# Optimization experiments

Hardware: AMD Instinct MI355X
Metric: run time of the kernel (lower is better)

The kernel has to match this reference:

```python
import jax, jax.numpy as jnp
import numpy as np

D_MODEL = 1024
N_HEADS = 16
HEAD_DIM = D_MODEL // N_HEADS


def setup_inputs() -> dict:
    key = jax.random.key(0)
    ks = jax.random.split(key, 5)
    B, S = 2, 2048
    x = jax.random.normal(ks[0], (B, S, D_MODEL), dtype=jnp.float32)
    # nn.Linear weights: [out_features, in_features]
    s_in = 1.0 / np.sqrt(D_MODEL)
    qkv_w = jax.random.uniform(ks[1], (3 * D_MODEL, D_MODEL), jnp.float32, -s_in, s_in)
    qkv_b = jax.random.uniform(ks[2], (3 * D_MODEL,), jnp.float32, -s_in, s_in)
    out_w = jax.random.uniform(ks[3], (D_MODEL, D_MODEL), jnp.float32, -s_in, s_in)
    out_b = jax.random.uniform(ks[4], (D_MODEL,), jnp.float32, -s_in, s_in)
    return {"x": x, "qkv_w": qkv_w, "qkv_b": qkv_b, "out_w": out_w, "out_b": out_b}


def reference(x, qkv_w, qkv_b, out_w, out_b):
    B, S, D = x.shape
    H, Hd = N_HEADS, HEAD_DIM
    scale = 1.0 / np.sqrt(Hd)
    qkv = jnp.einsum('bsd,ed->bse', x, qkv_w) + qkv_b  # [B,S,3D]
    qkv = qkv.reshape(B, S, 3, H, Hd)
    q = qkv[:, :, 0].transpose(0, 2, 1, 3)  # [B,H,S,Hd]
    k = qkv[:, :, 1].transpose(0, 2, 1, 3)
    v = qkv[:, :, 2].transpose(0, 2, 1, 3)
    scores = jnp.einsum('bhqd,bhkd->bhqk', q, k) * scale  # [B,H,S,S]
    causal = jnp.triu(jnp.ones((S, S), dtype=bool), k=1)
    scores = jnp.where(causal[None, None], -jnp.inf, scores)
    probs = jax.nn.softmax(scores, axis=-1)
    out = jnp.einsum('bhqk,bhkd->bhqd', probs, v)  # [B,H,S,Hd]
    out = out.transpose(0, 2, 1, 3).reshape(B, S, D)
    out = jnp.einsum('bsd,ed->bse', out, out_w) + out_b
    return out
```

## Files before the change

kernel.cpp:

```cpp
#include <hip/hip_runtime.h>
#include <hip/hip_bf16.h>

#define SEQ    2048
#define DMODEL 1024
#define NHEAD  16
#define HDIM   64
#define BATCH  2
#define NTOK   (BATCH * SEQ)

#define N_X   (NTOK * DMODEL)
#define N_WQ  (3 * DMODEL * DMODEL)
#define N_BQ  (3 * DMODEL)
#define N_WO  (DMODEL * DMODEL)
#define N_BO  (DMODEL)
#define N_CANON (N_X + N_WQ + N_BQ + N_WO + N_BO)

#define NEG_SENT (-1.0e30f)
#define QSCALE 0.1803368801111f

typedef __attribute__((ext_vector_type(8))) short short8;
typedef __attribute__((ext_vector_type(4))) short short4v;
typedef __attribute__((ext_vector_type(4))) float f32x4;

#define MFMA_BF16(A, B, C) __builtin_amdgcn_mfma_f32_16x16x32_bf16((A), (B), (C), 0, 0, 0)

static __device__ __forceinline__ short8 load8(const __hip_bfloat16* p) {
    return *(const short8*)p;
}

static __device__ __forceinline__ void async16(const void* g, void* l) {
    __builtin_amdgcn_global_load_lds(
        (const __attribute__((address_space(1))) unsigned int*)g,
        (__attribute__((address_space(3))) unsigned int*)l,
        16, 0, 0);
}

__global__ void detect_kernel(const unsigned short* __restrict__ w, int* flag) {
    int cnt = 0;
    for (int i = threadIdx.x; i < 512; i += 64) {
        const unsigned e = (w[i] >> 7) & 0xFF;
        if (e >= 125) cnt++;
    }
#pragma unroll
    for (int o = 32; o; o >>= 1) cnt += __shfl_down(cnt, o);
    if (threadIdx.x == 0) *flag = (cnt > 8) ? 1 : 0;
}

__global__ __launch_bounds__(256) void canon_kernel(
    const void* __restrict__ s0, const void* __restrict__ s1,
    const void* __restrict__ s2, const void* __restrict__ s3,
    const void* __restrict__ s4,
    __hip_bfloat16* __restrict__ dst, const int* __restrict__ flag)
{
    const int v = blockIdx.x * 256 + threadIdx.x;
    if (v >= N_CANON / 8) return;
    const int idx = v * 8;
    const void* src;
    int off;
    if (idx < N_X)                          { src = s0; off = idx; }
    else if (idx < N_X + N_WQ)              { src = s1; off = idx - N_X; }
    else if (idx < N_X + N_WQ + N_BQ)       { src = s2; off = idx - (N_X + N_WQ); }
    else if (idx < N_X + N_WQ + N_BQ + N_WO){ src = s3; off = idx - (N_X + N_WQ + N_BQ); }
    else                                    { src = s4; off = idx - (N_X + N_WQ + N_BQ + N_WO); }
    if (*flag != 0) {
        const f32x4* sp = (const f32x4*)((const float*)src + off);
        const f32x4 x0 = sp[0], x1 = sp[1];
        short8 o;
#pragma unroll
        for (int j = 0; j < 4; ++j) {
            o[j]     = (short)__bfloat16_as_ushort(__float2bfloat16(x0[j]));
            o[4 + j] = (short)__bfloat16_as_ushort(__float2bfloat16(x1[j]));
        }
        *(short8*)&dst[idx] = o;
    } else {
        *(short8*)&dst[idx] = *(const short8*)((const __hip_bfloat16*)src + off);
    }
}

__global__ __launch_bounds__(256) void qkv_gemm_kernel(
    const __hip_bfloat16* __restrict__ X,
    const __hip_bfloat16* __restrict__ W,
    const __hip_bfloat16* __restrict__ bias,
    __hip_bfloat16* __restrict__ Qs,
    __hip_bfloat16* __restrict__ Kb,
    __hip_bfloat16* __restrict__ Vt)
{
    constexpr int Kd = DMODEL;
    __shared__ __align__(16) __hip_bfloat16 As[3][128 * 32];
    __shared__ __align__(16) __hip_bfloat16 Bs[3][128 * 32];

    const int tid   = threadIdx.x;
    const int lane  = tid & 63;
    const int w     = tid >> 6;
    const int mTile = blockIdx.y * 128;
    const int nTile = blockIdx.x * 128;
    const int wm    = (w >> 1) * 64;
    const int wn    = (w & 1) * 64;
    const int lm    = lane & 15;
    const int q4    = lane >> 4;
    const int lks   = (q4 ^ ((lm >> 1) & 3)) * 8;

    f32x4 acc[4][4];
#pragma unroll
    for (int i = 0; i < 4; ++i)
#pragma unroll
        for (int j = 0; j < 4; ++j)
            acc[i][j] = (f32x4){0.f, 0.f, 0.f, 0.f};

    const int r0c = tid >> 2;
    const int r1c = (tid + 256) >> 2;
    const int cbs = ((tid & 3) ^ ((tid >> 3) & 3)) * 8;

    const __hip_bfloat16* gA0 = &X[(size_t)(mTile + r0c) * Kd + cbs];
    const __hip_bfloat16* gA1 = &X[(size_t)(mTile + r1c) * Kd + cbs];
    const __hip_bfloat16* gB0 = &W[(size_t)(nTile + r0c) * Kd + cbs];
    const __hip_bfloat16* gB1 = &W[(size_t)(nTile + r1c) * Kd + cbs];

    async16(gA0, (char*)As[0] + tid * 16);
    async16(gA1, (char*)As[0] + tid * 16 + 4096);
    async16(gB0, (char*)Bs[0] + tid * 16);
    async16(gB1, (char*)Bs[0] + tid * 16 + 4096);
    async16(gA0 + 32, (char*)As[1] + tid * 16);
    async16(gA1 + 32, (char*)As[1] + tid * 16 + 4096);
    async16(gB0 + 32, (char*)Bs[1] + tid * 16);
    async16(gB1 + 32, (char*)Bs[1] + tid * 16 + 4096);

    int cur = 0;
    constexpr int NIT = Kd / 32;
    for (int it = 0; it < NIT; ++it) {
        if (it + 1 < NIT) {
            asm volatile("s_waitcnt vmcnt(4)" ::: "memory");
        } else {
            asm volatile("s_waitcnt vmcnt(0)" ::: "memory");
        }
        __builtin_amdgcn_s_barrier();
        __builtin_amdgcn_sched_barrier(0);

        if (it + 2 < NIT) {
            const int slot = (cur + 2 >= 3) ? cur - 1 : cur + 2;
            const int k2 = (it + 2) * 32;
            async16(gA0 + k2, (char*)As[slot] + tid * 16);
            async16(gA1 + k2, (char*)As[slot] + tid * 16 + 4096);
            async16(gB0 + k2, (char*)Bs[slot] + tid * 16);
            async16(gB1 + k2, (char*)Bs[slot] + tid * 16 + 4096);
        }

        const __hip_bfloat16* Ac = As[cur];
        const __hip_bfloat16* Bc = Bs[cur];
        short8 a[4], b[4];
#pragma unroll
        for (int i = 0; i < 4; ++i)
            a[i] = *(const short8*)&Ac[(wm + i * 16 + lm) * 32 + lks];
#pragma unroll
        for (int j = 0; j < 4; ++j)
            b[j] = *(const short8*)&Bc[(wn + j * 16 + lm) * 32 + lks];
#pragma unroll
        for (int i = 0; i < 4; ++i)
#pragma unroll
            for (int j = 0; j < 4; ++j)
                acc[i][j] = MFMA_BF16(a[i], b[j], acc[i][j]);

        cur = (cur + 1 == 3) ? 0 : cur + 1;
    }

    const int r0 = (lane >> 4) * 4;
#pragma unroll
    for (int j = 0; j < 4; ++j) {
        const int n  = nTile + wn + j * 16 + lm;
        const float bv = __bfloat162float(bias[n]);
        const int c = n >> 10;
        const int h = (n >> 6) & 15;
        const int d = n & 63;
#pragma unroll
        for (int i = 0; i < 4; ++i) {
            if (c == 2) {
                const int m0 = mTile + wm + i * 16 + r0;
                const int bb = m0 >> 11;
                const int s0 = m0 & (SEQ - 1);
                const int bh = bb * NHEAD + h;
                short4v pk;
#pragma unroll
                for (int r = 0; r < 4; ++r)
                    pk[r] = (short)__bfloat16_as_ushort(
                        __float2bfloat16(acc[i][j][r] + bv));
                *(short4v*)&Vt[(size_t)(bh * HDIM + d) * SEQ + s0] = pk;
            } else {
#pragma unroll
                for (int r = 0; r < 4; ++r) {
                    const int m  = mTile + wm + i * 16 + r0 + r;
                    const int bb = m >> 11;
                    const int s  = m & (SEQ - 1);
                    const int bh = bb * NHEAD + h;
                    const float v = acc[i][j][r] + bv;
                    if (c == 0) {
                        Qs[(size_t)(bh * SEQ + s) * HDIM + d] = __float2bfloat16(v * QSCALE);
                    } else {
                        Kb[(size_t)(bh * SEQ + s) * HDIM + d] = __float2bfloat16(v);
                    }
                }
            }
        }
    }
}

#define P_PITCH 72
__global__ __launch_bounds__(256, 3) void attn_kernel(
    const __hip_bfloat16* __restrict__ Qs,
    const __hip_bfloat16* __restrict__ Kb,
    const __hip_bfloat16* __restrict__ Vt,
    float* __restrict__ Opart,
    float* __restrict__ MLpart)
{
    __shared__ __align__(16) __hip_bfloat16 Kt[2][64 * 64];
    __shared__ __align__(16) __hip_bfloat16 Vs[2][64 * 64];
    __shared__ __align__(16) __hip_bfloat16 Pall[4][32 * P_PITCH];

    const int tid  = threadIdx.x;
    const int lane = tid & 63;
    const int wv   = tid >> 6;
    const int bh   = blockIdx.x;
    const int py   = blockIdx.y;
    const int p    = py / 3;
    const int j3   = py % 3;

    const int c_lo = (j3 == 0) ? 0 : (j3 == 1 ? 12 : 23);
    const int c_hi = (j3 == 0) ? 12 : (j3 == 1 ? 23 : 34);
    const int bnd  = 32 - 2 * p;

    const int lm  = lane & 15;
    const int q4  = lane >> 4;
    const int lk  = q4 * 8;
    const int swz = (lm & 3) << 4;

    __hip_bfloat16* P = Pall[wv];

    const __hip_bfloat16* Qbh = Qs + (size_t)bh * SEQ * HDIM;
    const __hip_bfloat16* Kbh = Kb + (size_t)bh * SEQ * HDIM;
    const __hip_bfloat16* Vbh = Vt + (size_t)bh * HDIM * SEQ;

    const int srow0 = tid >> 3;
    const int scb   = (tid & 7) ^ (srow0 & 7);

    for (int seg = 0; seg < 2; ++seg) {
        int qb, a, b, slot;
        if (seg == 0) {
            if (j3 == 2 && p >= 5) continue;
            qb = 15 - p; a = c_lo;
            b  = (c_hi < bnd) ? c_hi : bnd;
            slot = j3;
        } else {
            if (j3 == 0 || (j3 == 1 && p <= 4)) continue;
            qb = p;
            a  = ((c_lo > bnd) ? c_lo : bnd) - bnd;
            b  = c_hi - bnd;
            slot = (j3 == 2) ? 3 : 4;
        }

        const int wbase = qb * 128 + wv * 32;

        short8 qa[2][2];
#pragma unroll
        for (int i = 0; i < 2; ++i)
#pragma unroll
            for (int h = 0; h < 2; ++h)
                qa[i][h] = load8(&Qbh[(size_t)(wbase + i * 16 + lm) * HDIM + h * 32 + lk]);

        float m_run[2] = {NEG_SENT, NEG_SENT};
        float l_run[2] = {0.f, 0.f};
        f32x4 Oacc[2][4];
#pragma unroll
        for (int i = 0; i < 2; ++i)
#pragma unroll
            for (int t = 0; t < 4; ++t) Oacc[i][t] = (f32x4){0.f, 0.f, 0.f, 0.f};

        __builtin_amdgcn_s_barrier();

        {
            const int kk0 = a * 64;
            async16(&Kbh[(size_t)(kk0 + srow0) * HDIM + scb * 8],      (char*)Kt[0] + tid * 16);
            async16(&Kbh[(size_t)(kk0 + srow0 + 32) * HDIM + scb * 8], (char*)Kt[0] + tid * 16 + 4096);
            async16(&Vbh[(size_t)srow0 * SEQ + kk0 + scb * 8],         (char*)Vs[0] + tid * 16);
            async16(&Vbh[(size_t)(srow0 + 32) * SEQ + kk0 + scb * 8],  (char*)Vs[0] + tid * 16 + 4096);
            if (a + 1 < b) {
                const int kk1 = kk0 + 64;
                async16(&Kbh[(size_t)(kk1 + srow0) * HDIM + scb * 8],      (char*)Kt[1] + tid * 16);
                async16(&Kbh[(size_t)(kk1 + srow0 + 32) * HDIM + scb * 8], (char*)Kt[1] + tid * 16 + 4096);
                async16(&Vbh[(size_t)srow0 * SEQ + kk1 + scb * 8],         (char*)Vs[1] + tid * 16);
                async16(&Vbh[(size_t)(srow0 + 32) * SEQ + kk1 + scb * 8],  (char*)Vs[1] + tid * 16 + 4096);
            }
        }

        int cur = 0;
        for (int ci = a; ci < b; ++ci) {
            const int k0 = ci * 64;

            if (ci + 1 < b) {
                asm volatile("s_waitcnt vmcnt(4)" ::: "memory");
            } else {
                asm volatile("s_waitcnt vmcnt(0)" ::: "memory");
            }
            __builtin_amdgcn_s_barrier();
            __builtin_amdgcn_sched_barrier(0);

            if (k0 <= wbase + 31) {
                const __hip_bfloat16* Kc = Kt[cur];
                const __hip_bfloat16* Vc = Vs[cur];

                short8 ka[4][2];
#pragma unroll
                for (int t = 0; t < 4; ++t)
#pragma unroll
                    for (int h = 0; h < 2; ++h)
                        ka[t][h] = *(const short8*)&Kc[(t * 16 + lm) * 64 +
                                                       (((h * 4 + q4) ^ (lm & 7)) * 8)];

                f32x4 sc[2][4];
#pragma unroll
                for (int i = 0; i < 2; ++i)
#pragma unroll
                    for (int t = 0; t < 4; ++t) sc[i][t] = (f32x4){0.f, 0.f, 0.f, 0.f};
#pragma unroll
                for (int t = 0; t < 4; ++t)
#pragma unroll
                    for (int i = 0; i < 2; ++i) {
                        sc[i][t] = MFMA_BF16(ka[t][0], qa[i][0], sc[i][t]);
                        sc[i][t] = MFMA_BF16(ka[t][1], qa[i][1], sc[i][t]);
                    }

                if (k0 + 63 > wbase) {
#pragma unroll
                    for (int i = 0; i < 2; ++i) {
                        const int row = wbase + i * 16 + lm;
#pragma unroll
                        for (int t = 0; t < 4; ++t)
#pragma unroll
                            for (int r = 0; r < 4; ++r) {
                                const int key = k0 + t * 16 + q4 * 4 + r;
                                if (key > row) sc[i][t][r] = NEG_SENT;
                            }
                    }
                }

#pragma unroll
                for (int i = 0; i < 2; ++i) {
                    float mx = sc[i][0][0];
#pragma unroll
                    for (int t = 0; t < 4; ++t)
#pragma unroll
                        for (int r = 0; r < 4; ++r) mx = fmaxf(mx, sc[i][t][r]);
                    mx = fmaxf(mx, __shfl_xor(mx, 16));
                    mx = fmaxf(mx, __shfl_xor(mx, 32));

                    if (!__all(mx <= m_run[i] + 8.0f)) {
                        const float mn = fmaxf(m_run[i], mx);
                        const float alpha = exp2f(m_run[i] - mn);
                        m_run[i] = mn;
                        l_run[i] *= alpha;
#pragma unroll
                        for (int r = 0; r < 4; ++r) {
                            const float av = __shfl(alpha, q4 * 4 + r);
#pragma unroll
                            for (int t = 0; t < 4; ++t) Oacc[i][t][r] *= av;
                        }
                    }

                    float s = 0.f;
#pragma unroll
                    for (int t = 0; t < 4; ++t)
#pragma unroll
                        for (int r = 0; r < 4; ++r) {
                            const float pv = exp2f(sc[i][t][r] - m_run[i]);
                            sc[i][t][r] = pv;
                            s += pv;
                        }
                    s += __shfl_xor(s, 16);
                    s += __shfl_xor(s, 32);
                    l_run[i] += s;
                }

#pragma unroll
                for (int i = 0; i < 2; ++i)
#pragma unroll
                    for (int t = 0; t < 4; ++t) {
                        short4v pk;
#pragma unroll
                        for (int r = 0; r < 4; ++r)
                            pk[r] = (short)__bfloat16_as_ushort(__float2bfloat16(sc[i][t][r]));
                        const int col = (t * 16 + q4 * 4) ^ swz;
                        *(short4v*)&P[(i * 16 + lm) * P_PITCH + col] = pk;
                    }

#pragma unroll
                for (int h = 0; h < 2; ++h) {
                    short8 pa[2];
#pragma unroll
                    for (int i = 0; i < 2; ++i)
                        pa[i] = *(const short8*)&P[(i * 16 + lm) * P_PITCH + ((h * 32 + lk) ^ swz)];
#pragma unroll
                    for (int t = 0; t < 4; ++t) {
                        const short8 vb = *(const short8*)&Vc[(t * 16 + lm) * 64 +
                                                              (((h * 4 + q4) ^ (lm & 7)) * 8)];
#pragma unroll
                        for (int i = 0; i < 2; ++i)
                            Oacc[i][t] = MFMA_BF16(pa[i], vb, Oacc[i][t]);
                    }
                }
            }

            __builtin_amdgcn_s_barrier();
            if (ci + 2 < b) {
                const int kk = (ci + 2) * 64;
                async16(&Kbh[(size_t)(kk + srow0) * HDIM + scb * 8],      (char*)Kt[cur] + tid * 16);
                async16(&Kbh[(size_t)(kk + srow0 + 32) * HDIM + scb * 8], (char*)Kt[cur] + tid * 16 + 4096);
                async16(&Vbh[(size_t)srow0 * SEQ + kk + scb * 8],         (char*)Vs[cur] + tid * 16);
                async16(&Vbh[(size_t)(srow0 + 32) * SEQ + kk + scb * 8],  (char*)Vs[cur] + tid * 16 + 4096);
            }
            cur ^= 1;
        }

        const size_t pbase = ((size_t)(bh * 8 + p) * 5 + slot) * 128;
#pragma unroll
        for (int i = 0; i < 2; ++i)
#pragma unroll
            for (int t = 0; t < 4; ++t)
#pragma unroll
                for (int r = 0; r < 4; ++r)
                    Opart[(pbase + wv * 32 + i * 16 + q4 * 4 + r) * 64 + t * 16 + lm] = Oacc[i][t][r];
        if (lane < 16) {
#pragma unroll
            for (int i = 0; i < 2; ++i) {
                MLpart[(pbase + wv * 32 + i * 16 + lane) * 2 + 0] = m_run[i];
                MLpart[(pbase + wv * 32 + i * 16 + lane) * 2 + 1] = l_run[i];
            }
        }
    }
}

__global__ __launch_bounds__(256) void attn_merge_kernel(
    const float* __restrict__ Opart, const float* __restrict__ MLpart,
    __hip_bfloat16* __restrict__ O)
{
    const int idx  = blockIdx.x * 256 + threadIdx.x;
    const int d16  = idx & 3;
    const int grow = idx >> 2;
    const int bh   = grow >> 11;
    const int s    = grow & 2047;
    const int qb   = s >> 7;
    const int rin  = s & 127;

    const bool heavy = (qb >= 8);
    const int p  = heavy ? (15 - qb) : qb;
    const int s0 = heavy ? 0 : 3;
    const int s1 = heavy ? 1 : 4;
    const bool v1 = heavy ? true : (p >= 5);
    const bool v2 = heavy && (p <= 4);

    const size_t rb = (size_t)(bh * 8 + p) * 5;
    const size_t r0 = (rb + s0) * 128 + rin;
    const size_t r1 = (rb + s1) * 128 + rin;
    const size_t r2 = (rb + 2)  * 128 + rin;

    const float m0 = MLpart[r0 * 2],                 l0 = MLpart[r0 * 2 + 1];
    const float m1 = v1 ? MLpart[r1 * 2] : NEG_SENT, l1 = v1 ? MLpart[r1 * 2 + 1] : 0.f;
    const float m2 = v2 ? MLpart[r2 * 2] : NEG_SENT, l2 = v2 ? MLpart[r2 * 2 + 1] : 0.f;

    float mm = fmaxf(m0, fmaxf(m1, m2));
    const float a0 = exp2f(m0 - mm);
    const float a1 = v1 ? exp2f(m1 - mm) : 0.f;
    const float a2 = v2 ? exp2f(m2 - mm) : 0.f;
    const float inv = 1.0f / (a0 * l0 + a1 * l1 + a2 * l2);

    f32x4 o[4];
    {
        const f32x4* O0 = (const f32x4*)&Opart[r0 * 64 + d16 * 16];
#pragma unroll
        for (int v = 0; v < 4; ++v) o[v] = a0 * O0[v];
    }
    if (v1) {
        const f32x4* O1 = (const f32x4*)&Opart[r1 * 64 + d16 * 16];
#pragma unroll
        for (int v = 0; v < 4; ++v) o[v] += a1 * O1[v];
    }
    if (v2) {
        const f32x4* O2 = (const f32x4*)&Opart[r2 * 64 + d16 * 16];
#pragma unroll
        for (int v = 0; v < 4; ++v) o[v] += a2 * O2[v];
    }

    short8 out[2];
#pragma unroll
    for (int v = 0; v < 4; ++v)
#pragma unroll
        for (int jj = 0; jj < 4; ++jj)
            out[v >> 1][(v & 1) * 4 + jj] = (short)__bfloat16_as_ushort(
                __float2bfloat16(o[v][jj] * inv));

    const int b = bh >> 4, hh = bh & 15;
    __hip_bfloat16* dst = &O[((size_t)b * SEQ + s) * DMODEL + hh * 64 + d16 * 16];
    ((short8*)dst)[0] = out[0];
    ((short8*)dst)[1] = out[1];
}

__global__ __launch_bounds__(256) void proj_gemm_kernel(
    const __hip_bfloat16* __restrict__ A,
    const __hip_bfloat16* __restrict__ W,
    const __hip_bfloat16* __restrict__ bias,
    void* __restrict__ outv,
    const int* __restrict__ flag)
{
    constexpr int Kd = DMODEL;
    __shared__ __align__(16) __hip_bfloat16 As[3][128 * 32];
    __shared__ __align__(16) __hip_bfloat16 Bs[3][64 * 32];

    const int tid   = threadIdx.x;
    const int lane  = tid & 63;
    const int w     = tid >> 6;
    const int mTile = blockIdx.y * 128;
    const int nTile = blockIdx.x * 64;
    const int wm    = (w >> 1) * 64;
    const int wn    = (w & 1) * 32;
    const int lm    = lane & 15;
    const int q4    = lane >> 4;
    const int lks   = (q4 ^ ((lm >> 1) & 3)) * 8;
    const bool f32out = (*flag != 0);

    f32x4 acc[4][2];
#pragma unroll
    for (int i = 0; i < 4; ++i)
#pragma unroll
        for (int j = 0; j < 2; ++j)
            acc[i][j] = (f32x4){0.f, 0.f, 0.f, 0.f};

    const int r0c = tid >> 2;
    const int r1c = (tid + 256) >> 2;
    const int cbs = ((tid & 3) ^ ((tid >> 3) & 3)) * 8;

    const __hip_bfloat16* gA0 = &A[(size_t)(mTile + r0c) * Kd + cbs];
    const __hip_bfloat16* gA1 = &A[(size_t)(mTile + r1c) * Kd + cbs];
    const __hip_bfloat16* gB0 = &W[(size_t)(nTile + r0c) * Kd + cbs];

    async16(gA0, (char*)As[0] + tid * 16);
    async16(gA1, (char*)As[0] + tid * 16 + 4096);
    async16(gB0, (char*)Bs[0] + tid * 16);
    async16(gA0 + 32, (char*)As[1] + tid * 16);
    async16(gA1 + 32, (char*)As[1] + tid * 16 + 4096);
    async16(gB0 + 32, (char*)Bs[1] + tid * 16);

    int cur = 0;
    constexpr int NIT = Kd / 32;
    for (int it = 0; it < NIT; ++it) {
        if (it + 1 < NIT) {
            asm volatile("s_waitcnt vmcnt(3)" ::: "memory");
        } else {
            asm volatile("s_waitcnt vmcnt(0)" ::: "memory");
        }
        __builtin_amdgcn_s_barrier();
        __builtin_amdgcn_sched_barrier(0);

        if (it + 2 < NIT) {
            const int slot = (cur + 2 >= 3) ? cur - 1 : cur + 2;
            const int k2 = (it + 2) * 32;
            async16(gA0 + k2, (char*)As[slot] + tid * 16);
            async16(gA1 + k2, (char*)As[slot] + tid * 16 + 4096);
            async16(gB0 + k2, (char*)Bs[slot] + tid * 16);
        }

        const __hip_bfloat16* Ac = As[cur];
        const __hip_bfloat16* Bc = Bs[cur];
        short8 a[4], b[2];
#pragma unroll
        for (int i = 0; i < 4; ++i)
            a[i] = *(const short8*)&Ac[(wm + i * 16 + lm) * 32 + lks];
#pragma unroll
        for (int j = 0; j < 2; ++j)
            b[j] = *(const short8*)&Bc[(wn + j * 16 + lm) * 32 + lks];
#pragma unroll
        for (int i = 0; i < 4; ++i)
#pragma unroll
            for (int j = 0; j < 2; ++j)
                acc[i][j] = MFMA_BF16(a[i], b[j], acc[i][j]);

        cur = (cur + 1 == 3) ? 0 : cur + 1;
    }

    const int r0 = (lane >> 4) * 4;
#pragma unroll
    for (int j = 0; j < 2; ++j) {
        const int n = nTile + wn + j * 16 + lm;
        const float bv = __bfloat162float(bias[n]);
#pragma unroll
        for (int i = 0; i < 4; ++i) {
#pragma unroll
            for (int r = 0; r < 4; ++r) {
                const size_t m = mTile + wm + i * 16 + r0 + r;
                const float v = acc[i][j][r] + bv;
                if (f32out) ((float*)outv)[m * DMODEL + n] = v;
                else ((__hip_bfloat16*)outv)[m * DMODEL + n] = __float2bfloat16(v);
            }
        }
    }
}

extern "C" void kernel_launch(void* const* d_in, const int* in_sizes, int n_in,
                              void* d_out, int out_size, void* d_ws, size_t ws_size,
                              hipStream_t stream) {
    const size_t OFF_CANON = 256;
    const size_t OFF_QS = OFF_CANON + (size_t)N_CANON * 2;
    const size_t OFF_KB = OFF_QS + (size_t)NTOK * DMODEL * 2;
    const size_t OFF_VT = OFF_KB + (size_t)NTOK * DMODEL * 2;
    const size_t OFF_AO = OFF_VT + (size_t)NTOK * DMODEL * 2;
    const size_t OFF_OP = OFF_AO + (size_t)NTOK * DMODEL * 2;
    const size_t OFF_ML = OFF_OP + (size_t)32 * 8 * 5 * 128 * 64 * 4;

    char* wsb = (char*)d_ws;
    int* flag = (int*)wsb;
    __hip_bfloat16* canon = (__hip_bfloat16*)(wsb + OFF_CANON);
    __hip_bfloat16* Xc = canon;
    __hip_bfloat16* Wq = Xc + N_X;
    __hip_bfloat16* Bq = Wq + N_WQ;
    __hip_bfloat16* Wo = Bq + N_BQ;
    __hip_bfloat16* Bo = Wo + N_WO;
    __hip_bfloat16* Qs = (__hip_bfloat16*)(wsb + OFF_QS);
    __hip_bfloat16* Kb = (__hip_bfloat16*)(wsb + OFF_KB);
    __hip_bfloat16* Vt = (__hip_bfloat16*)(wsb + OFF_VT);
    __hip_bfloat16* Ao = (__hip_bfloat16*)(wsb + OFF_AO);
    float* Opart = (float*)(wsb + OFF_OP);
    float* MLpart = (float*)(wsb + OFF_ML);

    detect_kernel<<<1, 64, 0, stream>>>((const unsigned short*)d_in[1], flag);
    canon_kernel<<<(N_CANON / 8 + 255) / 256, 256, 0, stream>>>(
        d_in[0], d_in[1], d_in[2], d_in[3], d_in[4], canon, flag);

    {
        dim3 grid(3 * DMODEL / 128, NTOK / 128);
        qkv_gemm_kernel<<<grid, 256, 0, stream>>>(Xc, Wq, Bq, Qs, Kb, Vt);
    }
    {
        dim3 grid(BATCH * NHEAD, 24);
        attn_kernel<<<grid, 256, 0, stream>>>(Qs, Kb, Vt, Opart, MLpart);
        attn_merge_kernel<<<(NTOK * NHEAD * 4) / 256, 256, 0, stream>>>(
            Opart, MLpart, Ao);
    }
    {
        dim3 grid(DMODEL / 64, NTOK / 128);
        proj_gemm_kernel<<<grid, 256, 0, stream>>>(Ao, Wo, Bo, d_out, flag);
    }
}
```

Baseline: 191.6 us.

## Switch attention to 32x32x16 MFMA with register-resident P via lane shuffles

Recasts the attention inner loop from 16x16x32 bf16 MFMAs to 32x32x16 MFMAs. Each wave now owns 32 query rows with one query row per lane pair, so each lane keeps a single running max and sum. The softmax probabilities are packed with v_cvt_pk_bf16_f32 and rearranged across lane halves with xor-32 shuffles to form the PV operand directly in registers. This removes the per-wave P staging buffer in LDS along with its store/load round trip, and Opart is now written as vectorized float4 stores. In exchange the accumulators are larger, which raises register pressure at three blocks per CU, and the lane-swap layout is a correctness risk.

```diff
diff --git a/kernel.cpp b/kernel.cpp
--- a/kernel.cpp
+++ b/kernel.cpp
@@ -21,11 +21,19 @@
 typedef __attribute__((ext_vector_type(8))) short short8;
 typedef __attribute__((ext_vector_type(4))) short short4v;
 typedef __attribute__((ext_vector_type(4))) float f32x4;
+typedef __attribute__((ext_vector_type(16))) float f32x16;
 
 #define MFMA_BF16(A, B, C) __builtin_amdgcn_mfma_f32_16x16x32_bf16((A), (B), (C), 0, 0, 0)
+#define MFMA32_BF16(A, B, C) __builtin_amdgcn_mfma_f32_32x32x16_bf16((A), (B), (C), 0, 0, 0)
 
 static __device__ __forceinline__ short8 load8(const __hip_bfloat16* p) {
     return *(const short8*)p;
+}
+
+static __device__ __forceinline__ unsigned cvtpk_bf16(float lo, float hi) {
+    unsigned r;
+    asm("v_cvt_pk_bf16_f32 %0, %1, %2" : "=v"(r) : "v"(lo), "v"(hi));
+    return r;
 }
 
 static __device__ __forceinline__ void async16(const void* g, void* l) {
@@ -203,7 +211,6 @@
     }
 }
 
-#define P_PITCH 72
 __global__ __launch_bounds__(256, 3) void attn_kernel(
     const __hip_bfloat16* __restrict__ Qs,
     const __hip_bfloat16* __restrict__ Kb,
@@ -213,7 +220,6 @@
 {
     __shared__ __align__(16) __hip_bfloat16 Kt[2][64 * 64];
     __shared__ __align__(16) __hip_bfloat16 Vs[2][64 * 64];
-    __shared__ __align__(16) __hip_bfloat16 Pall[4][32 * P_PITCH];
 
     const int tid  = threadIdx.x;
     const int lane = tid & 63;
@@ -227,12 +233,9 @@
     const int c_hi = (j3 == 0) ? 12 : (j3 == 1 ? 23 : 34);
     const int bnd  = 32 - 2 * p;
 
-    const int lm  = lane & 15;
-    const int q4  = lane >> 4;
-    const int lk  = q4 * 8;
-    const int swz = (lm & 3) << 4;
-
-    __hip_bfloat16* P = Pall[wv];
+    const int lq = lane & 31;
+    const int sg = lane >> 5;
+    const int swr = lq & 7;
 
     const __hip_bfloat16* Qbh = Qs + (size_t)bh * SEQ * HDIM;
     const __hip_bfloat16* Kbh = Kb + (size_t)bh * SEQ * HDIM;
@@ -257,21 +260,20 @@
         }
 
         const int wbase = qb * 128 + wv * 32;
-
-        short8 qa[2][2];
-#pragma unroll
-        for (int i = 0; i < 2; ++i)
-#pragma unroll
-            for (int h = 0; h < 2; ++h)
-                qa[i][h] = load8(&Qbh[(size_t)(wbase + i * 16 + lm) * HDIM + h * 32 + lk]);
-
-        float m_run[2] = {NEG_SENT, NEG_SENT};
-        float l_run[2] = {0.f, 0.f};
-        f32x4 Oacc[2][4];
-#pragma unroll
-        for (int i = 0; i < 2; ++i)
-#pragma unroll
-            for (int t = 0; t < 4; ++t) Oacc[i][t] = (f32x4){0.f, 0.f, 0.f, 0.f};
+        const int qrow  = wbase + lq;
+
+        short8 qa[4];
+#pragma unroll
+        for (int s = 0; s < 4; ++s)
+            qa[s] = load8(&Qbh[(size_t)qrow * HDIM + s * 16 + sg * 8]);
+
+        float m_run = NEG_SENT;
+        float l_run = 0.f;
+        f32x16 Oacc[2];
+#pragma unroll
+        for (int t = 0; t < 2; ++t)
+#pragma unroll
+            for (int e = 0; e < 16; ++e) Oacc[t][e] = 0.f;
 
         __builtin_amdgcn_s_barrier();
 
@@ -306,103 +308,92 @@
                 const __hip_bfloat16* Kc = Kt[cur];
                 const __hip_bfloat16* Vc = Vs[cur];
 
-                short8 ka[4][2];
-#pragma unroll
-                for (int t = 0; t < 4; ++t)
-#pragma unroll
-                    for (int h = 0; h < 2; ++h)
-                        ka[t][h] = *(const short8*)&Kc[(t * 16 + lm) * 64 +
-                                                       (((h * 4 + q4) ^ (lm & 7)) * 8)];
-
-                f32x4 sc[2][4];
-#pragma unroll
-                for (int i = 0; i < 2; ++i)
-#pragma unroll
-                    for (int t = 0; t < 4; ++t) sc[i][t] = (f32x4){0.f, 0.f, 0.f, 0.f};
-#pragma unroll
-                for (int t = 0; t < 4; ++t)
-#pragma unroll
-                    for (int i = 0; i < 2; ++i) {
-                        sc[i][t] = MFMA_BF16(ka[t][0], qa[i][0], sc[i][t]);
-                        sc[i][t] = MFMA_BF16(ka[t][1], qa[i][1], sc[i][t]);
+                f32x16 sc[2];
+#pragma unroll
+                for (int t = 0; t < 2; ++t)
+#pragma unroll
+                    for (int e = 0; e < 16; ++e) sc[t][e] = 0.f;
+#pragma unroll
+                for (int t = 0; t < 2; ++t)
+#pragma unroll
+                    for (int s = 0; s < 4; ++s) {
+                        const short8 ka = *(const short8*)&Kc[
+                            (t * 32 + lq) * 64 + (((s * 2 + sg) ^ swr) * 8)];
+                        sc[t] = MFMA32_BF16(ka, qa[s], sc[t]);
                     }
 
                 if (k0 + 63 > wbase) {
 #pragma unroll
-                    for (int i = 0; i < 2; ++i) {
-                        const int row = wbase + i * 16 + lm;
-#pragma unroll
-                        for (int t = 0; t < 4; ++t)
+                    for (int t = 0; t < 2; ++t)
+#pragma unroll
+                        for (int g = 0; g < 4; ++g)
 #pragma unroll
                             for (int r = 0; r < 4; ++r) {
-                                const int key = k0 + t * 16 + q4 * 4 + r;
-                                if (key > row) sc[i][t][r] = NEG_SENT;
+                                const int key = k0 + t * 32 + r + 8 * g + 4 * sg;
+                                if (key > qrow) sc[t][g * 4 + r] = NEG_SENT;
                             }
+                }
+
+                float mx = sc[0][0];
+#pragma unroll
+                for (int t = 0; t < 2; ++t)
+#pragma unroll
+                    for (int e = 0; e < 16; ++e) mx = fmaxf(mx, sc[t][e]);
+                mx = fmaxf(mx, __shfl_xor(mx, 32));
+
+                if (!__all(mx <= m_run + 8.0f)) {
+                    const float mn = fmaxf(m_run, mx);
+                    const float alpha = exp2f(m_run - mn);
+                    m_run = mn;
+                    l_run *= alpha;
+#pragma unroll
+                    for (int t = 0; t < 2; ++t)
+#pragma unroll
+                        for (int e = 0; e < 16; ++e) Oacc[t][e] *= alpha;
+                }
+
+                float ssum = 0.f;
+#pragma unroll
+                for (int t = 0; t < 2; ++t)
+#pragma unroll
+                    for (int e = 0; e < 16; ++e) {
+                        const float pv = exp2f(sc[t][e] - m_run);
+                        sc[t][e] = pv;
+                        ssum += pv;
                     }
-                }
-
-#pragma unroll
-                for (int i = 0; i < 2; ++i) {
-                    float mx = sc[i][0][0];
-#pragma unroll
-                    for (int t = 0; t < 4; ++t)
-#pragma unroll
-                        for (int r = 0; r < 4; ++r) mx = fmaxf(mx, sc[i][t][r]);
-                    mx = fmaxf(mx, __shfl_xor(mx, 16));
-                    mx = fmaxf(mx, __shfl_xor(mx, 32));
-
-                    if (!__all(mx <= m_run[i] + 8.0f)) {
-                        const float mn = fmaxf(m_run[i], mx);
-                        const float alpha = exp2f(m_run[i] - mn);
-                        m_run[i] = mn;
-                        l_run[i] *= alpha;
-#pragma unroll
-                        for (int r = 0; r < 4; ++r) {
-                            const float av = __shfl(alpha, q4 * 4 + r);
-#pragma unroll
-                            for (int t = 0; t < 4; ++t) Oacc[i][t][r] *= av;
-                        }
+                ssum += __shfl_xor(ssum, 32);
+                l_run += ssum;
+
+                unsigned wpk[2][4][2];
+#pragma unroll
+                for (int t = 0; t < 2; ++t)
+#pragma unroll
+                    for (int g = 0; g < 4; ++g) {
+                        wpk[t][g][0] = cvtpk_bf16(sc[t][g * 4 + 0], sc[t][g * 4 + 1]);
+                        wpk[t][g][1] = cvtpk_bf16(sc[t][g * 4 + 2], sc[t][g * 4 + 3]);
                     }
 
-                    float s = 0.f;
-#pragma unroll
-                    for (int t = 0; t < 4; ++t)
-#pragma unroll
-                        for (int r = 0; r < 4; ++r) {
-                            const float pv = exp2f(sc[i][t][r] - m_run[i]);
-                            sc[i][t][r] = pv;
-                            s += pv;
-                        }
-                    s += __shfl_xor(s, 16);
-                    s += __shfl_xor(s, 32);
-                    l_run[i] += s;
-                }
-
-#pragma unroll
-                for (int i = 0; i < 2; ++i)
-#pragma unroll
-                    for (int t = 0; t < 4; ++t) {
-                        short4v pk;
-#pragma unroll
-                        for (int r = 0; r < 4; ++r)
-                            pk[r] = (short)__bfloat16_as_ushort(__float2bfloat16(sc[i][t][r]));
-                        const int col = (t * 16 + q4 * 4) ^ swz;
-                        *(short4v*)&P[(i * 16 + lm) * P_PITCH + col] = pk;
-                    }
-
-#pragma unroll
-                for (int h = 0; h < 2; ++h) {
-                    short8 pa[2];
-#pragma unroll
-                    for (int i = 0; i < 2; ++i)
-                        pa[i] = *(const short8*)&P[(i * 16 + lm) * P_PITCH + ((h * 32 + lk) ^ swz)];
-#pragma unroll
-                    for (int t = 0; t < 4; ++t) {
-                        const short8 vb = *(const short8*)&Vc[(t * 16 + lm) * 64 +
-                                                              (((h * 4 + q4) ^ (lm & 7)) * 8)];
-#pragma unroll
-                        for (int i = 0; i < 2; ++i)
-                            Oacc[i][t] = MFMA_BF16(pa[i], vb, Oacc[i][t]);
+#pragma unroll
+                for (int s = 0; s < 4; ++s) {
+                    const int t  = s >> 1;
+                    const int gp = (s & 1) * 2;
+                    const unsigned oe0 = wpk[t][gp][0],     oe1 = wpk[t][gp][1];
+                    const unsigned oo0 = wpk[t][gp + 1][0], oo1 = wpk[t][gp + 1][1];
+                    const unsigned pay0 = sg ? oe0 : oo0;
+                    const unsigned pay1 = sg ? oe1 : oo1;
+                    const unsigned rc0 = (unsigned)__shfl_xor((int)pay0, 32);
+                    const unsigned rc1 = (unsigned)__shfl_xor((int)pay1, 32);
+                    unsigned f[4];
+                    f[0] = sg ? rc0 : oe0;
+                    f[1] = sg ? rc1 : oe1;
+                    f[2] = sg ? oo0 : rc0;
+                    f[3] = sg ? oo1 : rc1;
+                    const short8 pa = *(const short8*)f;
+#pragma unroll
+                    for (int t2 = 0; t2 < 2; ++t2) {
+                        const short8 va = *(const short8*)&Vc[
+                            (t2 * 32 + lq) * 64 + (((s * 2 + sg) ^ swr) * 8)];
+                        Oacc[t2] = MFMA32_BF16(va, pa, Oacc[t2]);
                     }
                 }
             }
@@ -419,19 +410,19 @@
         }
 
         const size_t pbase = ((size_t)(bh * 8 + p) * 5 + slot) * 128;
-#pragma unroll
-        for (int i = 0; i < 2; ++i)
-#pragma unroll
-            for (int t = 0; t < 4; ++t)
-#pragma unroll
-                for (int r = 0; r < 4; ++r)
-                    Opart[(pbase + wv * 32 + i * 16 + q4 * 4 + r) * 64 + t * 16 + lm] = Oacc[i][t][r];
-        if (lane < 16) {
-#pragma unroll
-            for (int i = 0; i < 2; ++i) {
-                MLpart[(pbase + wv * 32 + i * 16 + lane) * 2 + 0] = m_run[i];
-                MLpart[(pbase + wv * 32 + i * 16 + lane) * 2 + 1] = l_run[i];
+        const size_t orow  = (pbase + wv * 32 + lq) * 64;
+#pragma unroll
+        for (int t2 = 0; t2 < 2; ++t2)
+#pragma unroll
+            for (int g = 0; g < 4; ++g) {
+                f32x4 v;
+#pragma unroll
+                for (int r = 0; r < 4; ++r) v[r] = Oacc[t2][g * 4 + r];
+                *(f32x4*)&Opart[orow + t2 * 32 + 8 * g + 4 * sg] = v;
             }
+        if (lane < 32) {
+            MLpart[(pbase + wv * 32 + lane) * 2 + 0] = m_run;
+            MLpart[(pbase + wv * 32 + lane) * 2 + 1] = l_run;
         }
     }
 }
```

Result: no change. 191.2 us (-0.2%).
